# Optimization experiments

Measured on AMD Instinct MI355X. Metric: run time of the kernel, lower is better.

The kernel has to match this reference:

```python
import jax, jax.numpy as jnp
import numpy as np
import math

D_MODEL = 2048
N_HEADS = 16
D_K = D_MODEL // N_HEADS  # 128
B = 2
L = 2048


def _rope_cos_sin(seq_len, d_k, dtype):
    inv_freq = 1.0 / (10000.0 ** (jnp.arange(0, d_k, 2, dtype=jnp.float32) / d_k))
    t = jnp.arange(seq_len, dtype=jnp.float32)
    freqs = jnp.outer(t, inv_freq)  # [L, d_k//2]
    return jnp.cos(freqs).astype(dtype), jnp.sin(freqs).astype(dtype)


def _apply_rope(x, cos, sin):
    # x: [B, H, L, d_k]; cos/sin: [L, d_k//2] broadcast over B,H
    half = x.shape[-1] // 2
    x1, x2 = x[..., :half], x[..., half:]
    c = cos[None, None, :, :]
    s = sin[None, None, :, :]
    return jnp.concatenate([x1 * c - x2 * s, x1 * s + x2 * c], axis=-1)


def setup_inputs() -> dict:
    key = jax.random.key(0)
    ks = jax.random.split(key, 8)
    scale = 1.0 / math.sqrt(D_MODEL)
    query = jax.random.normal(ks[0], (B, L, D_MODEL), dtype=jnp.float32)
    k_in = jax.random.normal(ks[1], (B, L, D_MODEL), dtype=jnp.float32)
    v_in = jax.random.normal(ks[2], (B, L, D_MODEL), dtype=jnp.float32)
    w_q = jax.random.normal(ks[3], (D_MODEL, D_MODEL), dtype=jnp.float32) * scale
    w_k = jax.random.normal(ks[4], (D_MODEL, D_MODEL), dtype=jnp.float32) * scale
    w_v = jax.random.normal(ks[5], (D_MODEL, D_MODEL), dtype=jnp.float32) * scale
    w_o = jax.random.normal(ks[6], (D_MODEL, D_MODEL), dtype=jnp.float32) * scale
    mask = jnp.tril(jnp.ones((L, L), dtype=bool))[None, None, :, :]
    return {"query": query, "key": k_in, "value": v_in, "mask": mask,
            "w_q": w_q, "w_k": w_k, "w_v": w_v, "w_o": w_o}


def reference(query, key, value, mask, w_q, w_k, w_v, w_o):
    Bq, Lq, D = query.shape
    Lk = key.shape[1]
    # Linear (no bias): y = x @ W.T ; split heads -> [B, H, L, d_k]
    def proj(x, w, length):
        y = jnp.einsum('bld,ed->ble', x, w)
        return y.reshape(x.shape[0], length, N_HEADS, D_K).transpose(0, 2, 1, 3)
    Q = proj(query, w_q, Lq)
    K = proj(key, w_k, Lk)
    V = proj(value, w_v, Lk)
    cos_q, sin_q = _rope_cos_sin(Lq, D_K, query.dtype)
    cos_k, sin_k = _rope_cos_sin(Lk, D_K, key.dtype)
    Q = _apply_rope(Q, cos_q, sin_q)
    K = _apply_rope(K, cos_k, sin_k)
    scores = jnp.einsum('bhqd,bhkd->bhqk', Q, K) / math.sqrt(D_K)
    neg = jnp.finfo(scores.dtype).min
    scores = jnp.where(mask, scores, neg)
    attn = jax.nn.softmax(scores, axis=-1)
    out = jnp.einsum('bhqk,bhkd->bhqd', attn, V)
    out = out.transpose(0, 2, 1, 3).reshape(Bq, Lq, D)
    return jnp.einsum('bld,ed->ble', out, w_o)
```

## Files before the change

kernel.cpp:

```cpp
#include <hip/hip_runtime.h>
#include <stdint.h>

#define L_SEQ 2048
#define DMODEL 2048
#define NHEADS 16
#define DK 128
#define BATCH 2
#define MROWS (BATCH*L_SEQ)

typedef float f32x4 __attribute__((ext_vector_type(4)));
typedef short s16x8 __attribute__((ext_vector_type(8)));
typedef unsigned short u16;
typedef unsigned int u32;

__device__ __forceinline__ u16 f2bf(float f){
  u32 u = __builtin_bit_cast(u32, f);
  u += 0x7fffu + ((u >> 16) & 1u);
  return (u16)(u >> 16);
}
__device__ __forceinline__ float bf2f(u16 h){
  u32 u = ((u32)h) << 16;
  return __builtin_bit_cast(float, u);
}
__device__ __forceinline__ void gload_lds16(const void* g, void* l){
  __builtin_amdgcn_global_load_lds((const __attribute__((address_space(1))) void*)g,
                                   (__attribute__((address_space(3))) void*)l, 16, 0, 0);
}

__global__ void k_cvt_all(const float* __restrict__ s0, const float* __restrict__ s1,
                          const float* __restrict__ s2, const float* __restrict__ s3,
                          const float* __restrict__ s4, const float* __restrict__ s5,
                          const float* __restrict__ s6,
                          u16* __restrict__ d0, u16* __restrict__ d1, u16* __restrict__ d2,
                          u16* __restrict__ d3, u16* __restrict__ d4, u16* __restrict__ d5,
                          u16* __restrict__ d6){
  const int XC = MROWS*DMODEL/8;
  const int WC = DMODEL*DMODEL/8;
  const int total = 3*XC + 4*WC;
  int stride = gridDim.x * blockDim.x;
  for (int i = blockIdx.x*blockDim.x + threadIdx.x; i < total; i += stride){
    const float* s; u16* d; int j;
    if (i < XC)        { s=s0; d=d0; j=i; }
    else if (i < 2*XC) { s=s1; d=d1; j=i-XC; }
    else if (i < 3*XC) { s=s2; d=d2; j=i-2*XC; }
    else {
      int k2 = i - 3*XC; int wi = k2 / WC; j = k2 - wi*WC;
      s = wi==0?s3 : wi==1?s4 : wi==2?s5 : s6;
      d = wi==0?d3 : wi==1?d4 : wi==2?d5 : d6;
    }
    const f32x4* sp = (const f32x4*)s + (size_t)j*2;
    f32x4 a = sp[0], b = sp[1];
    s16x8 o;
    o[0]=(short)f2bf(a[0]); o[1]=(short)f2bf(a[1]); o[2]=(short)f2bf(a[2]); o[3]=(short)f2bf(a[3]);
    o[4]=(short)f2bf(b[0]); o[5]=(short)f2bf(b[1]); o[6]=(short)f2bf(b[2]); o[7]=(short)f2bf(b[3]);
    ((s16x8*)d)[j] = o;
  }
}

__global__ void k_tab(float* __restrict__ ct, float* __restrict__ st){
  int idx = blockIdx.x*blockDim.x + threadIdx.x;
  int l = idx >> 6, i = idx & 63;
  float e = (float)i * (1.0f/64.0f);
  float inv = 1.0f / powf(10000.0f, e);
  float fr = (float)l * inv;
  ct[idx] = cosf(fr);
  st[idx] = sinf(fr);
}

__global__ void k_rope2(u16* __restrict__ xq, u16* __restrict__ xk,
                        const float* __restrict__ ct, const float* __restrict__ st){
  int t0 = blockIdx.x*blockDim.x + threadIdx.x;
  u16* x = (t0 & (1<<19)) ? xk : xq;
  int t = t0 & ((1<<19)-1);
  int i8  = (t & 7) * 8;
  int h   = (t >> 3) & 15;
  int row = t >> 7;
  int l   = row & (L_SEQ-1);
  u16* p = x + (size_t)row*DMODEL + h*DK;
  s16x8 a  = *(s16x8*)(p + i8);
  s16x8 bq = *(s16x8*)(p + 64 + i8);
  const float* cp = ct + l*64 + i8;
  const float* sp = st + l*64 + i8;
  f32x4 c0 = *(const f32x4*)cp, c1 = *(const f32x4*)(cp+4);
  f32x4 s0 = *(const f32x4*)sp, s1 = *(const f32x4*)(sp+4);
  float cc[8] = {c0[0],c0[1],c0[2],c0[3],c1[0],c1[1],c1[2],c1[3]};
  float ss[8] = {s0[0],s0[1],s0[2],s0[3],s1[0],s1[1],s1[2],s1[3]};
  s16x8 y1, y2;
  #pragma unroll
  for (int e=0;e<8;e++){
    float x1 = bf2f((u16)a[e]), x2 = bf2f((u16)bq[e]);
    y1[e] = (short)f2bf(x1*cc[e] - x2*ss[e]);
    y2[e] = (short)f2bf(x1*ss[e] + x2*cc[e]);
  }
  *(s16x8*)(p + i8)      = y1;
  *(s16x8*)(p + 64 + i8) = y2;
}

__global__ __launch_bounds__(256)
void k_gemm3(const u16* __restrict__ A0, const u16* __restrict__ A1, const u16* __restrict__ A2,
             const u16* __restrict__ B0, const u16* __restrict__ B1, const u16* __restrict__ B2,
             u16* __restrict__ C0, u16* __restrict__ C1, u16* __restrict__ C2){
  __shared__ u16 As[128*64];
  __shared__ u16 Bs[128*64];
  const int z = blockIdx.z;
  const u16* __restrict__ A  = z==0?A0 : z==1?A1 : A2;
  const u16* __restrict__ Bw = z==0?B0 : z==1?B1 : B2;
  u16* __restrict__ Cb       = z==0?C0 : z==1?C1 : C2;
  const int tid = threadIdx.x, w = tid>>6, l = tid&63;
  const int lg = l>>4, lr = l&15;
  const int lin = (int)blockIdx.y*16 + (int)blockIdx.x;
  const int lin2 = (lin&7)*64 + (lin>>3);
  const int bm = (lin2>>4)*128, bn = (lin2&15)*128;
  const int K = DMODEL, N = DMODEL;
  f32x4 acc[4][4];
  #pragma unroll
  for (int i=0;i<4;i++)
    #pragma unroll
    for (int j=0;j<4;j++) acc[i][j] = (f32x4){0.f,0.f,0.f,0.f};

  const int chunkbase = w*64 + l;
  const int wm = (w>>1)*64, wn = (w&1)*64;

  for (int k0 = 0; k0 < K; k0 += 64){
    __syncthreads();
    #pragma unroll
    for (int i=0;i<4;i++){
      int chunk = i*256 + chunkbase;
      int row = chunk >> 3;
      int cbs = ((chunk&7)<<4) ^ ((row&7)<<4);
      const u16* ga = A  + (size_t)(bm+row)*K + k0 + (cbs>>1);
      const u16* gb = Bw + (size_t)(bn+row)*K + k0 + (cbs>>1);
      gload_lds16(ga, (void*)&As[(i*256 + w*64)*8]);
      gload_lds16(gb, (void*)&Bs[(i*256 + w*64)*8]);
    }
    __syncthreads();
    #pragma unroll
    for (int kc=0; kc<2; kc++){
      s16x8 af[4], bfr[4];
      #pragma unroll
      for (int mi=0; mi<4; mi++){
        int row = wm + mi*16 + lr;
        int off = row*128 + ((kc*64 + lg*16) ^ ((row&7)<<4));
        af[mi] = *(const s16x8*)((const char*)As + off);
      }
      #pragma unroll
      for (int ni=0; ni<4; ni++){
        int row = wn + ni*16 + lr;
        int off = row*128 + ((kc*64 + lg*16) ^ ((row&7)<<4));
        bfr[ni] = *(const s16x8*)((const char*)Bs + off);
      }
      #pragma unroll
      for (int mi=0; mi<4; mi++)
        #pragma unroll
        for (int ni=0; ni<4; ni++)
          acc[mi][ni] = __builtin_amdgcn_mfma_f32_16x16x32_bf16(af[mi], bfr[ni], acc[mi][ni], 0,0,0);
    }
  }
  #pragma unroll
  for (int mi=0; mi<4; mi++)
    #pragma unroll
    for (int ni=0; ni<4; ni++)
      #pragma unroll
      for (int r=0; r<4; r++){
        int row = bm + wm + mi*16 + (lg<<2) + r;
        int col = bn + wn + ni*16 + lr;
        Cb[(size_t)row*N + col] = f2bf(acc[mi][ni][r]);
      }
}

__global__ __launch_bounds__(256)
void k_gemm(const u16* __restrict__ A, const u16* __restrict__ Bw,
            float* __restrict__ Cf){
  __shared__ u16 As[128*64];
  __shared__ u16 Bs[128*64];
  const int tid = threadIdx.x, w = tid>>6, l = tid&63;
  const int lg = l>>4, lr = l&15;
  const int lin = (int)blockIdx.y*16 + (int)blockIdx.x;
  const int lin2 = (lin&7)*64 + (lin>>3);
  const int bm = (lin2>>4)*128, bn = (lin2&15)*128;
  const int K = DMODEL, N = DMODEL;
  f32x4 acc[4][4];
  #pragma unroll
  for (int i=0;i<4;i++)
    #pragma unroll
    for (int j=0;j<4;j++) acc[i][j] = (f32x4){0.f,0.f,0.f,0.f};

  const int chunkbase = w*64 + l;
  const int wm = (w>>1)*64, wn = (w&1)*64;

  for (int k0 = 0; k0 < K; k0 += 64){
    __syncthreads();
    #pragma unroll
    for (int i=0;i<4;i++){
      int chunk = i*256 + chunkbase;
      int row = chunk >> 3;
      int cbs = ((chunk&7)<<4) ^ ((row&7)<<4);
      const u16* ga = A  + (size_t)(bm+row)*K + k0 + (cbs>>1);
      const u16* gb = Bw + (size_t)(bn+row)*K + k0 + (cbs>>1);
      gload_lds16(ga, (void*)&As[(i*256 + w*64)*8]);
      gload_lds16(gb, (void*)&Bs[(i*256 + w*64)*8]);
    }
    __syncthreads();
    #pragma unroll
    for (int kc=0; kc<2; kc++){
      s16x8 af[4], bfr[4];
      #pragma unroll
      for (int mi=0; mi<4; mi++){
        int row = wm + mi*16 + lr;
        int off = row*128 + ((kc*64 + lg*16) ^ ((row&7)<<4));
        af[mi] = *(const s16x8*)((const char*)As + off);
      }
      #pragma unroll
      for (int ni=0; ni<4; ni++){
        int row = wn + ni*16 + lr;
        int off = row*128 + ((kc*64 + lg*16) ^ ((row&7)<<4));
        bfr[ni] = *(const s16x8*)((const char*)Bs + off);
      }
      #pragma unroll
      for (int mi=0; mi<4; mi++)
        #pragma unroll
        for (int ni=0; ni<4; ni++)
          acc[mi][ni] = __builtin_amdgcn_mfma_f32_16x16x32_bf16(af[mi], bfr[ni], acc[mi][ni], 0,0,0);
    }
  }
  #pragma unroll
  for (int mi=0; mi<4; mi++)
    #pragma unroll
    for (int ni=0; ni<4; ni++)
      #pragma unroll
      for (int r=0; r<4; r++){
        int row = bm + wm + mi*16 + (lg<<2) + r;
        int col = bn + wn + ni*16 + lr;
        Cf[(size_t)row*N + col] = acc[mi][ni][r];
      }
}

__global__ __launch_bounds__(256)
void k_attn(const u16* __restrict__ Qp, const u16* __restrict__ Kp,
            const u16* __restrict__ Vp, u16* __restrict__ AO){
  __shared__ u16 Ks[2][64*128];
  __shared__ u16 Vs[128*64];
  __shared__ u16 Ps[4][16*72];
  const int tid = threadIdx.x, w = tid>>6, l = tid&63;
  const int lg = l>>4, lr = l&15;
  const int lin = (int)blockIdx.y * (int)gridDim.x + (int)blockIdx.x;
  const int xcd = lin & 7, s8 = lin >> 3;
  const int bh  = xcd*4 + (s8 >> 4);
  const int qtp = s8 & 15;
  const int b = bh>>4, h = bh&15;
  const size_t kvbase = (size_t)(b*L_SEQ)*DMODEL + h*DK;
  const float scale = 0.08838834764831845f;

  u32 vv[2][8];

  auto issueK = [&](int j, int buf){
    #pragma unroll
    for (int i=0;i<4;i++){
      int chunk = i*256 + w*64 + l;
      int row = chunk >> 4;
      int cb = ((chunk&15)<<4) ^ ((row&7)<<4);
      const u16* src = Kp + kvbase + (size_t)(j*64 + row)*DMODEL + (cb>>1);
      gload_lds16(src, (void*)&Ks[buf][(i*256 + w*64)*8]);
    }
  };
  auto issueV = [&](int j){
    #pragma unroll
    for (int it=0; it<2; it++){
      int task = it*256 + tid;
      int dp = task & 63, kb = task >> 6;
      const u16* vsrc = Vp + kvbase + (size_t)(j*64 + kb*8)*DMODEL + dp*2;
      #pragma unroll
      for (int e=0;e<8;e++) vv[it][e] = *(const u32*)(vsrc + (size_t)e*DMODEL);
    }
  };
  auto writeV = [&](){
    #pragma unroll
    for (int it=0; it<2; it++){
      int task = it*256 + tid;
      int dp = task & 63, kb = task >> 6;
      int d0 = dp*2;
      s16x8 lo, hi;
      #pragma unroll
      for (int e=0;e<8;e++){ lo[e] = (short)(vv[it][e] & 0xffffu); hi[e] = (short)(vv[it][e] >> 16); }
      int g = ((d0>>1)&7)<<4;
      *(s16x8*)((char*)&Vs[0] + d0*128     + ((kb*16) ^ g)) = lo;
      *(s16x8*)((char*)&Vs[0] + (d0+1)*128 + ((kb*16) ^ g)) = hi;
    }
  };

  for (int half=0; half<2; half++){
    const int qt = half==0 ? qtp : 31-qtp;
    if (half) __syncthreads();

    s16x8 qf[4];
    {
      const u16* qptr = Qp + (size_t)(b*L_SEQ + qt*64 + w*16 + lr)*DMODEL + h*DK + lg*8;
      #pragma unroll
      for (int kc=0; kc<4; kc++) qf[kc] = *(const s16x8*)(qptr + kc*32);
    }
    f32x4 o[8];
    #pragma unroll
    for (int dt=0; dt<8; dt++) o[dt] = (f32x4){0.f,0.f,0.f,0.f};
    float mrow[4] = {-1e30f,-1e30f,-1e30f,-1e30f};
    float lrow[4] = {0.f,0.f,0.f,0.f};

    issueK(0, 0);
    issueV(0);

    for (int j=0; j<=qt; j++){
      const int cur = j & 1;
      asm volatile("s_waitcnt vmcnt(16)" ::: "memory");
      __builtin_amdgcn_sched_barrier(0);
      __builtin_amdgcn_s_barrier();
      __builtin_amdgcn_sched_barrier(0);
      if (j < qt) issueK(j+1, cur^1);

      f32x4 st4[4];
      __builtin_amdgcn_s_setprio(1);
      #pragma unroll
      for (int ni=0; ni<4; ni++){
        f32x4 a = (f32x4){0.f,0.f,0.f,0.f};
        #pragma unroll
        for (int kc=0; kc<4; kc++){
          int row = ni*16 + lr;
          int off = row*256 + ((kc*64 + lg*16) ^ ((row&7)<<4));
          s16x8 kf = *(const s16x8*)((const char*)&Ks[cur][0] + off);
          a = __builtin_amdgcn_mfma_f32_16x16x32_bf16(qf[kc], kf, a, 0,0,0);
        }
        st4[ni] = a;
      }
      __builtin_amdgcn_s_setprio(0);

      float sv[4][4], tmax[4];
      const bool diag = (j == qt);
      #pragma unroll
      for (int r=0;r<4;r++){
        float mx = -1e30f;
        #pragma unroll
        for (int ni=0;ni<4;ni++){
          float x = st4[ni][r]*scale;
          if (diag){
            int kg = ni*16 + lr;
            int qg = w*16 + lg*4 + r;
            if (kg > qg) x = -1e30f;
          }
          sv[ni][r] = x;
          mx = fmaxf(mx, x);
        }
        tmax[r] = mx;
      }
      #pragma unroll
      for (int r=0;r<4;r++){
        #pragma unroll
        for (int msk=1; msk<16; msk<<=1) tmax[r] = fmaxf(tmax[r], __shfl_xor(tmax[r], msk, 64));
        float mn = fmaxf(mrow[r], tmax[r]);
        float al = __expf(mrow[r]-mn);
        mrow[r] = mn;
        float ps = 0.f;
        #pragma unroll
        for (int ni=0;ni<4;ni++){
          float p = __expf(sv[ni][r]-mn);
          ps += p;
          Ps[w][(lg*4 + r)*72 + ni*16 + lr] = f2bf(p);
        }
        #pragma unroll
        for (int msk=1; msk<16; msk<<=1) ps += __shfl_xor(ps, msk, 64);
        lrow[r] = al*lrow[r] + ps;
        #pragma unroll
        for (int dt=0;dt<8;dt++) o[dt][r] *= al;
      }
      s16x8 pa[2];
      #pragma unroll
      for (int kc=0;kc<2;kc++) pa[kc] = *(const s16x8*)(&Ps[w][lr*72 + kc*32 + lg*8]);

      if (j < qt){ asm volatile("s_waitcnt vmcnt(4)" ::: "memory"); }
      else       { asm volatile("s_waitcnt vmcnt(0)" ::: "memory"); }
      __builtin_amdgcn_sched_barrier(0);
      writeV();
      if (j < qt) issueV(j+1);
      asm volatile("s_waitcnt lgkmcnt(0)" ::: "memory");
      __builtin_amdgcn_sched_barrier(0);
      __builtin_amdgcn_s_barrier();
      __builtin_amdgcn_sched_barrier(0);

      __builtin_amdgcn_s_setprio(1);
      #pragma unroll
      for (int dt=0;dt<8;dt++){
        #pragma unroll
        for (int kc=0;kc<2;kc++){
          int d = dt*16 + lr;
          int off = d*128 + ((kc*64 + lg*16) ^ (((d>>1)&7)<<4));
          s16x8 vf = *(const s16x8*)((const char*)&Vs[0] + off);
          o[dt] = __builtin_amdgcn_mfma_f32_16x16x32_bf16(pa[kc], vf, o[dt], 0,0,0);
        }
      }
      __builtin_amdgcn_s_setprio(0);
    }

    #pragma unroll
    for (int r=0;r<4;r++){
      float inv = 1.0f / lrow[r];
      size_t rowg = (size_t)(b*L_SEQ + qt*64 + w*16 + lg*4 + r);
      #pragma unroll
      for (int dt=0;dt<8;dt++)
        AO[rowg*DMODEL + h*DK + dt*16 + lr] = f2bf(o[dt][r]*inv);
    }
  }
}

extern "C" void kernel_launch(void* const* d_in, const int* in_sizes, int n_in,
                              void* d_out, int out_size, void* d_ws, size_t ws_size,
                              hipStream_t stream){
  const float* q  = (const float*)d_in[0];
  const float* k  = (const float*)d_in[1];
  const float* v  = (const float*)d_in[2];
  const float* wq = (const float*)d_in[4];
  const float* wk = (const float*)d_in[5];
  const float* wv = (const float*)d_in[6];
  const float* wo = (const float*)d_in[7];
  (void)in_sizes; (void)n_in; (void)out_size; (void)ws_size;

  const size_t MD = (size_t)MROWS*DMODEL;
  const size_t DD = (size_t)DMODEL*DMODEL;
  char* ws = (char*)d_ws;
  size_t off = 0;
  auto alloc = [&](size_t bytes)->void*{ void* p = ws + off; off += (bytes + 255) & ~(size_t)255; return p; };
  u16* Xq = (u16*)alloc(MD*2);
  u16* Xk = (u16*)alloc(MD*2);
  u16* Xv = (u16*)alloc(MD*2);
  u16* Wq = (u16*)alloc(DD*2);
  u16* Wk = (u16*)alloc(DD*2);
  u16* Wv = (u16*)alloc(DD*2);
  u16* Wo = (u16*)alloc(DD*2);
  u16* Qp = (u16*)alloc(MD*2);
  u16* Kp = (u16*)alloc(MD*2);
  u16* Vp = (u16*)alloc(MD*2);
  float* ct = (float*)alloc((size_t)L_SEQ*64*4);
  float* st = (float*)alloc((size_t)L_SEQ*64*4);
  u16* AO = Xq;

  k_cvt_all<<<2048,256,0,stream>>>(q, k, v, wq, wk, wv, wo,
                                   Xq, Xk, Xv, Wq, Wk, Wv, Wo);
  k_tab<<<512,256,0,stream>>>(ct, st);

  k_gemm3<<<dim3(16,32,3),256,0,stream>>>(Xq, Xk, Xv, Wq, Wk, Wv, Qp, Kp, Vp);
  k_rope2<<<4096,256,0,stream>>>(Qp, Kp, ct, st);
  k_attn<<<dim3(16,32),256,0,stream>>>(Qp, Kp, Vp, AO);
  k_gemm<<<dim3(16,32),256,0,stream>>>(AO, Wo, (float*)d_out);
}
```

Measured before the change: 304.0 us.

## Compute softmax row sums via MFMA and skip rescaling when max barely changes

The running softmax denominator is now accumulated by an extra MFMA that multiplies the bf16 probability tile by a vector of ones, replacing the per-row sum and its cross-lane shuffle reduction. The max update and output rescale are skipped when every lane's tile max stays within 8 of the current row max, a wave-uniform check, so the max shuffles and alpha multiplies run only when needed. The denominator now sums bf16-rounded probabilities, which matches what the PV product uses. It costs two extra MFMAs per tile and one more accumulator register set.

```diff
diff --git a/kernel.cpp b/kernel.cpp
--- a/kernel.cpp
+++ b/kernel.cpp
@@ -252,6 +252,9 @@
   const float scale = 0.08838834764831845f;
 
   u32 vv[2][8];
+  s16x8 ones;
+  #pragma unroll
+  for (int e=0;e<8;e++) ones[e] = (short)0x3F80;
 
   auto issueK = [&](int j, int buf){
     #pragma unroll
@@ -298,11 +301,10 @@
       #pragma unroll
       for (int kc=0; kc<4; kc++) qf[kc] = *(const s16x8*)(qptr + kc*32);
     }
-    f32x4 o[8];
-    #pragma unroll
-    for (int dt=0; dt<8; dt++) o[dt] = (f32x4){0.f,0.f,0.f,0.f};
+    f32x4 o[9];
+    #pragma unroll
+    for (int dt=0; dt<9; dt++) o[dt] = (f32x4){0.f,0.f,0.f,0.f};
     float mrow[4] = {-1e30f,-1e30f,-1e30f,-1e30f};
-    float lrow[4] = {0.f,0.f,0.f,0.f};
 
     issueK(0, 0);
     issueV(0);
@@ -331,11 +333,11 @@
       }
       __builtin_amdgcn_s_setprio(0);
 
-      float sv[4][4], tmax[4];
+      float sv[4][4];
+      float lanemax = -1e30f;
       const bool diag = (j == qt);
       #pragma unroll
       for (int r=0;r<4;r++){
-        float mx = -1e30f;
         #pragma unroll
         for (int ni=0;ni<4;ni++){
           float x = st4[ni][r]*scale;
@@ -345,29 +347,30 @@
             if (kg > qg) x = -1e30f;
           }
           sv[ni][r] = x;
-          mx = fmaxf(mx, x);
+          lanemax = fmaxf(lanemax, x);
         }
-        tmax[r] = mx;
+      }
+      float mmin = fminf(fminf(mrow[0],mrow[1]), fminf(mrow[2],mrow[3]));
+      if (!__all(lanemax <= mmin + 8.0f)){
+        #pragma unroll
+        for (int r=0;r<4;r++){
+          float tm = fmaxf(fmaxf(sv[0][r],sv[1][r]), fmaxf(sv[2][r],sv[3][r]));
+          #pragma unroll
+          for (int msk=1; msk<16; msk<<=1) tm = fmaxf(tm, __shfl_xor(tm, msk, 64));
+          float mn = fmaxf(mrow[r], tm);
+          float al = __expf(mrow[r]-mn);
+          mrow[r] = mn;
+          #pragma unroll
+          for (int dt=0;dt<9;dt++) o[dt][r] *= al;
+        }
       }
       #pragma unroll
       for (int r=0;r<4;r++){
         #pragma unroll
-        for (int msk=1; msk<16; msk<<=1) tmax[r] = fmaxf(tmax[r], __shfl_xor(tmax[r], msk, 64));
-        float mn = fmaxf(mrow[r], tmax[r]);
-        float al = __expf(mrow[r]-mn);
-        mrow[r] = mn;
-        float ps = 0.f;
-        #pragma unroll
         for (int ni=0;ni<4;ni++){
-          float p = __expf(sv[ni][r]-mn);
-          ps += p;
+          float p = __expf(sv[ni][r]-mrow[r]);
           Ps[w][(lg*4 + r)*72 + ni*16 + lr] = f2bf(p);
         }
-        #pragma unroll
-        for (int msk=1; msk<16; msk<<=1) ps += __shfl_xor(ps, msk, 64);
-        lrow[r] = al*lrow[r] + ps;
-        #pragma unroll
-        for (int dt=0;dt<8;dt++) o[dt][r] *= al;
       }
       s16x8 pa[2];
       #pragma unroll
@@ -394,12 +397,14 @@
           o[dt] = __builtin_amdgcn_mfma_f32_16x16x32_bf16(pa[kc], vf, o[dt], 0,0,0);
         }
       }
+      o[8] = __builtin_amdgcn_mfma_f32_16x16x32_bf16(pa[0], ones, o[8], 0,0,0);
+      o[8] = __builtin_amdgcn_mfma_f32_16x16x32_bf16(pa[1], ones, o[8], 0,0,0);
       __builtin_amdgcn_s_setprio(0);
     }
 
     #pragma unroll
     for (int r=0;r<4;r++){
-      float inv = 1.0f / lrow[r];
+      float inv = 1.0f / o[8][r];
       size_t rowg = (size_t)(b*L_SEQ + qt*64 + w*16 + lg*4 + r);
       #pragma unroll
       for (int dt=0;dt<8;dt++)
```

Result: faster. 275.0 us (-9.5%).
